# Optimization experiments

Hardware: AMD Instinct MI355X
Metric: run time of the kernel (lower is better)

## Reference

```python
import jax, jax.numpy as jnp
import numpy as np
from jax import lax

EPS = 1e-6

def setup_inputs() -> dict:
    key = jax.random.key(0)
    B, C, K, T = 32, 1, 128, 8000
    x = jax.random.uniform(key, (B, C, K, T), dtype=jnp.float32)
    # parameters exactly as in PCENLayer.__init__ (log of init values)
    log_s = jnp.full((1, 1, K), np.log(0.025), dtype=jnp.float32)
    log_alpha = jnp.full((1, 1, K, 1), np.log(0.8), dtype=jnp.float32)
    log_delta = jnp.full((1, 1, K, 1), np.log(10.0), dtype=jnp.float32)
    log_r = jnp.full((1, 1, K, 1), np.log(0.25), dtype=jnp.float32)
    return {"x": x, "log_s": log_s, "log_alpha": log_alpha,
            "log_delta": log_delta, "log_r": log_r}

def reference(x, log_s, log_alpha, log_delta, log_r):
    # x: [B, C, K, T]
    s = jax.nn.sigmoid(log_s)            # (1, 1, K) smoother coefficient
    init = x[..., 0]                     # init smoother from first frame

    def step(prev, xt):
        f = (1.0 - s) * prev + s * xt
        return f, f

    xs = jnp.moveaxis(x[..., 1:], -1, 0)             # (T-1, B, C, K)
    _, fs = lax.scan(step, init, xs)                 # (T-1, B, C, K)
    filtered = jnp.concatenate([init[None], fs], 0)  # (T, B, C, K)
    filtered = jnp.moveaxis(filtered, 0, -1)         # (B, C, K, T)

    alpha = jnp.exp(log_alpha)           # (1, 1, K, 1)
    delta = jnp.exp(log_delta)
    r = jnp.exp(log_r)
    return (x / (EPS + filtered) ** alpha + delta) ** r - delta ** r
```

## Files before the change

kernel.cpp:

```cpp
#include <hip/hip_runtime.h>
#include <math.h>


constexpr int   T_LEN = 8000;
constexpr int   CHUNK = 8;
constexpr int   NTH   = 1024;
constexpr int   NWAVE = NTH / 64;
constexpr int   NACT  = T_LEN / CHUNK;
constexpr int   KDIM  = 128;
constexpr float EPS_F = 1e-6f;

__global__ __launch_bounds__(NTH, 8) void pcen_kernel(
    const float* __restrict__ x,
    const float* __restrict__ log_s,
    const float* __restrict__ log_alpha,
    const float* __restrict__ log_delta,
    const float* __restrict__ log_r,
    float* __restrict__ out)
{
    __shared__ float wAs[NWAVE], wBs[NWAVE];

    const int seq  = blockIdx.x;
    const int k    = seq % KDIM;
    const int tid  = threadIdx.x;
    const int lane = tid & 63;
    const int wave = tid >> 6;

    const float s       = 1.0f / (1.0f + expf(-log_s[k]));
    const float a       = 1.0f - s;
    const float alpha   = expf(log_alpha[k]);
    const float delta   = expf(log_delta[k]);
    const float r       = expf(log_r[k]);
    const float delta_r = exp2f(r * __log2f(delta));

    const float* xp = x   + (size_t)seq * T_LEN + tid * CHUNK;
    float*       op = out + (size_t)seq * T_LEN + tid * CHUNK;
    const bool active = tid < NACT;

    float xv[CHUNK];
    if (active) {
        float4 v0 = ((const float4*)xp)[0];
        float4 v1 = ((const float4*)xp)[1];
        xv[0] = v0.x; xv[1] = v0.y; xv[2] = v0.z; xv[3] = v0.w;
        xv[4] = v1.x; xv[5] = v1.y; xv[6] = v1.z; xv[7] = v1.w;
    }

    float q[CHUNK];
    float A = 1.0f, B = 0.0f;
    if (active) {
        float f;
        if (tid == 0) {
            f = xv[0]; q[0] = f;
            #pragma unroll
            for (int j = 1; j < CHUNK; ++j) { f = fmaf(a, f, s * xv[j]); q[j] = f; }
            A = 0.0f;
        } else {
            f = 0.0f;
            #pragma unroll
            for (int j = 0; j < CHUNK; ++j) { f = fmaf(a, f, s * xv[j]); q[j] = f; }
            const float a2 = a * a, a4 = a2 * a2;
            A = a4 * a4;
        }
        B = f;
    }

    #pragma unroll
    for (int off = 1; off < 64; off <<= 1) {
        const float pA = __shfl_up(A, off, 64);
        const float pB = __shfl_up(B, off, 64);
        if (lane >= off) {
            B = fmaf(A, pB, B);
            A = A * pA;
        }
    }

    if (lane == 63) { wAs[wave] = A; wBs[wave] = B; }
    __syncthreads();
    if (wave == 0) {
        float cA = (lane < NWAVE) ? wAs[lane] : 1.0f;
        float cB = (lane < NWAVE) ? wBs[lane] : 0.0f;
        #pragma unroll
        for (int off = 1; off < NWAVE; off <<= 1) {
            const float pA = __shfl_up(cA, off, 64);
            const float pB = __shfl_up(cB, off, 64);
            if (lane >= off) {
                cB = fmaf(cA, pB, cB);
                cA = cA * pA;
            }
        }
        if (lane < NWAVE - 1) { wAs[lane + 1] = cA; wBs[lane + 1] = cB; }
        if (lane == 0)        { wAs[0] = 1.0f;      wBs[0] = 0.0f;      }
    }
    __syncthreads();

    float eA = __shfl_up(A, 1, 64);
    float eB = __shfl_up(B, 1, 64);
    if (lane == 0) { eA = 1.0f; eB = 0.0f; }
    float fin = fmaf(eA, wBs[wave], eB);
    if (tid == 0) fin = 0.0f;

    if (active) {
        float pw = a;
        #pragma unroll
        for (int j = 0; j < CHUNK; ++j) {
            const float f   = fmaf(pw, fin, q[j]);
            pw *= a;
            const float lg  = __log2f(EPS_F + f);
            const float inv = exp2f(-alpha * lg);
            const float u   = fmaf(xv[j], inv, delta);
            xv[j] = exp2f(r * __log2f(u)) - delta_r;
        }
        ((float4*)op)[0] = make_float4(xv[0], xv[1], xv[2], xv[3]);
        ((float4*)op)[1] = make_float4(xv[4], xv[5], xv[6], xv[7]);
    }
}

extern "C" void kernel_launch(void* const* d_in, const int* in_sizes, int n_in,
                              void* d_out, int out_size, void* d_ws, size_t ws_size,
                              hipStream_t stream) {
    const float* x         = (const float*)d_in[0];
    const float* log_s     = (const float*)d_in[1];
    const float* log_alpha = (const float*)d_in[2];
    const float* log_delta = (const float*)d_in[3];
    const float* log_r     = (const float*)d_in[4];
    float* out = (float*)d_out;

    const int nseq = in_sizes[0] / T_LEN;
    pcen_kernel<<<nseq, NTH, 0, stream>>>(x, log_s, log_alpha, log_delta, log_r, out);
}
```

Baseline: 238.0 us.

## Use 16-element chunks with 512 threads, raw exp2/log intrinsics, nontemporal stores

Each thread now handles 16 timesteps and blocks use 512 threads instead of 1024, which shortens the cross-thread scan. The recurrence is rescaled so the per-step multiply by s is dropped and s is applied once during output. The exp and log calls are replaced by the raw amdgcn exp2 and log intrinsics, and the output is written with nontemporal stores. Register pressure per thread rises, and the raw intrinsics skip denormal handling.

```diff
diff --git a/kernel.cpp b/kernel.cpp
--- a/kernel.cpp
+++ b/kernel.cpp
@@ -3,12 +3,15 @@
 
 
 constexpr int   T_LEN = 8000;
-constexpr int   CHUNK = 8;
-constexpr int   NTH   = 1024;
+constexpr int   CHUNK = 16;
+constexpr int   NTH   = 512;
 constexpr int   NWAVE = NTH / 64;
 constexpr int   NACT  = T_LEN / CHUNK;
 constexpr int   KDIM  = 128;
 constexpr float EPS_F = 1e-6f;
+constexpr float LOG2E = 1.4426950408889634f;
+
+typedef float f32x4 __attribute__((ext_vector_type(4)));
 
 __global__ __launch_bounds__(NTH, 8) void pcen_kernel(
     const float* __restrict__ x,
@@ -21,17 +24,20 @@
     __shared__ float wAs[NWAVE], wBs[NWAVE];
 
     const int seq  = blockIdx.x;
-    const int k    = seq % KDIM;
+    const int k    = seq & (KDIM - 1);
     const int tid  = threadIdx.x;
     const int lane = tid & 63;
     const int wave = tid >> 6;
 
-    const float s       = 1.0f / (1.0f + expf(-log_s[k]));
-    const float a       = 1.0f - s;
-    const float alpha   = expf(log_alpha[k]);
-    const float delta   = expf(log_delta[k]);
-    const float r       = expf(log_r[k]);
-    const float delta_r = exp2f(r * __log2f(delta));
+    const float ls      = log_s[k];
+    const float e_ns    = __builtin_amdgcn_exp2f(-ls * LOG2E);
+    const float inv_s   = 1.0f + e_ns;
+    const float s       = 1.0f / inv_s;
+    const float a       = e_ns * s;
+    const float alpha   = __builtin_amdgcn_exp2f(log_alpha[k] * LOG2E);
+    const float delta   = __builtin_amdgcn_exp2f(log_delta[k] * LOG2E);
+    const float r       = __builtin_amdgcn_exp2f(log_r[k] * LOG2E);
+    const float delta_r = __builtin_amdgcn_exp2f(r * log_delta[k] * LOG2E);
 
     const float* xp = x   + (size_t)seq * T_LEN + tid * CHUNK;
     float*       op = out + (size_t)seq * T_LEN + tid * CHUNK;
@@ -39,29 +45,31 @@
 
     float xv[CHUNK];
     if (active) {
-        float4 v0 = ((const float4*)xp)[0];
-        float4 v1 = ((const float4*)xp)[1];
-        xv[0] = v0.x; xv[1] = v0.y; xv[2] = v0.z; xv[3] = v0.w;
-        xv[4] = v1.x; xv[5] = v1.y; xv[6] = v1.z; xv[7] = v1.w;
+        #pragma unroll
+        for (int v = 0; v < CHUNK / 4; ++v) {
+            f32x4 t = ((const f32x4*)xp)[v];
+            xv[4*v+0] = t[0]; xv[4*v+1] = t[1];
+            xv[4*v+2] = t[2]; xv[4*v+3] = t[3];
+        }
     }
 
     float q[CHUNK];
     float A = 1.0f, B = 0.0f;
     if (active) {
-        float f;
+        float g;
         if (tid == 0) {
-            f = xv[0]; q[0] = f;
+            g = xv[0] * inv_s; q[0] = g;
             #pragma unroll
-            for (int j = 1; j < CHUNK; ++j) { f = fmaf(a, f, s * xv[j]); q[j] = f; }
+            for (int j = 1; j < CHUNK; ++j) { g = fmaf(a, g, xv[j]); q[j] = g; }
             A = 0.0f;
         } else {
-            f = 0.0f;
+            g = 0.0f;
             #pragma unroll
-            for (int j = 0; j < CHUNK; ++j) { f = fmaf(a, f, s * xv[j]); q[j] = f; }
-            const float a2 = a * a, a4 = a2 * a2;
-            A = a4 * a4;
+            for (int j = 0; j < CHUNK; ++j) { g = fmaf(a, g, xv[j]); q[j] = g; }
+            const float a2 = a * a, a4 = a2 * a2, a8 = a4 * a4;
+            A = a8 * a8;
         }
-        B = f;
+        B = g;
     }
 
     #pragma unroll
@@ -103,15 +111,20 @@
         float pw = a;
         #pragma unroll
         for (int j = 0; j < CHUNK; ++j) {
-            const float f   = fmaf(pw, fin, q[j]);
+            const float g   = fmaf(pw, fin, q[j]);
             pw *= a;
-            const float lg  = __log2f(EPS_F + f);
-            const float inv = exp2f(-alpha * lg);
+            const float lg  = __builtin_amdgcn_logf(fmaf(s, g, EPS_F));
+            const float inv = __builtin_amdgcn_exp2f(-alpha * lg);
             const float u   = fmaf(xv[j], inv, delta);
-            xv[j] = exp2f(r * __log2f(u)) - delta_r;
+            xv[j] = __builtin_amdgcn_exp2f(r * __builtin_amdgcn_logf(u)) - delta_r;
         }
-        ((float4*)op)[0] = make_float4(xv[0], xv[1], xv[2], xv[3]);
-        ((float4*)op)[1] = make_float4(xv[4], xv[5], xv[6], xv[7]);
+        #pragma unroll
+        for (int v = 0; v < CHUNK / 4; ++v) {
+            f32x4 t;
+            t[0] = xv[4*v+0]; t[1] = xv[4*v+1];
+            t[2] = xv[4*v+2]; t[3] = xv[4*v+3];
+            __builtin_nontemporal_store(t, ((f32x4*)op) + v);
+        }
     }
 }
 
```

Measured after the change: 396.1 us. 66.5% more time.
